# Performance work log

Hardware: AMD Instinct MI355X
Metric: run time of the kernel (lower is better)

## Reference

```python
import jax, jax.numpy as jnp
from jax import lax
import numpy as np

EPS = 1e-5
COMMITMENT = 0.25


def conv1d(x, w, b, pad):
    # x: [N,C,T], w: [O,I,K]
    y = lax.conv_general_dilated(x, w, window_strides=(1,), padding=[(pad, pad)],
                                 dimension_numbers=('NCH', 'OIH', 'NCH'))
    return y + b[None, :, None]


def batchnorm(x, g, b):
    # training-mode BN (PyTorch default): batch stats over (N, T), biased var
    m = jnp.mean(x, axis=(0, 2), keepdims=True)
    v = jnp.var(x, axis=(0, 2), keepdims=True)
    return (x - m) * lax.rsqrt(v + EPS) * g[None, :, None] + b[None, :, None]


def setup_inputs() -> dict:
    key = jax.random.key(0)
    ks = jax.random.split(key, 16)
    B, C_in, T = 16, 80, 4096
    H1, H2, D, K = 128, 256, 64, 512
    s = 0.05
    inp = {
        'x': jax.random.normal(ks[0], (B, C_in, T), jnp.float32),
        # encoder
        'enc_w1': jax.random.normal(ks[1], (H1, C_in, 3), jnp.float32) * s,
        'enc_b1': jnp.zeros((H1,), jnp.float32),
        'bn1_g': jnp.ones((H1,), jnp.float32), 'bn1_b': jnp.zeros((H1,), jnp.float32),
        'enc_w2': jax.random.normal(ks[2], (H2, H1, 3), jnp.float32) * s,
        'enc_b2': jnp.zeros((H2,), jnp.float32),
        'bn2_g': jnp.ones((H2,), jnp.float32), 'bn2_b': jnp.zeros((H2,), jnp.float32),
        'enc_w3': jax.random.normal(ks[3], (D, H2, 1), jnp.float32) * s,
        'enc_b3': jnp.zeros((D,), jnp.float32),
        # codebook, init uniform(-1/K, 1/K) like the torch module
        'codebook': jax.random.uniform(ks[4], (K, D), jnp.float32, -1.0 / K, 1.0 / K),
        # decoder (hidden_dims reversed: [256, 128])
        'dec_w1': jax.random.normal(ks[5], (H2, D, 3), jnp.float32) * s,
        'dec_b1': jnp.zeros((H2,), jnp.float32),
        'dbn1_g': jnp.ones((H2,), jnp.float32), 'dbn1_b': jnp.zeros((H2,), jnp.float32),
        'dec_w2': jax.random.normal(ks[6], (H1, H2, 3), jnp.float32) * s,
        'dec_b2': jnp.zeros((H1,), jnp.float32),
        'dbn2_g': jnp.ones((H1,), jnp.float32), 'dbn2_b': jnp.zeros((H1,), jnp.float32),
        'dec_w3': jax.random.normal(ks[7], (C_in, H1, 3), jnp.float32) * s,
        'dec_b3': jnp.zeros((C_in,), jnp.float32),
    }
    return inp


def _vqvae(x, enc_w1, enc_b1, bn1_g, bn1_b, enc_w2, enc_b2, bn2_g, bn2_b,
           enc_w3, enc_b3, codebook, dec_w1, dec_b1, dbn1_g, dbn1_b,
           dec_w2, dec_b2, dbn2_g, dbn2_b, dec_w3, dec_b3):
    # ---- Encoder ----
    h = jax.nn.relu(batchnorm(conv1d(x, enc_w1, enc_b1, 1), bn1_g, bn1_b))
    h = jax.nn.relu(batchnorm(conv1d(h, enc_w2, enc_b2, 1), bn2_g, bn2_b))
    z = conv1d(h, enc_w3, enc_b3, 0)  # [B, D, T]

    # ---- Vector Quantizer ----
    B, D, T = z.shape
    zt = jnp.transpose(z, (0, 2, 1))            # [B, T, D]
    flat = zt.reshape(-1, D)                    # [B*T, D]
    # squared L2 distances to codebook [B*T, K]
    d2 = (jnp.sum(flat * flat, axis=1, keepdims=True)
          + jnp.sum(codebook * codebook, axis=1)
          - 2.0 * flat @ codebook.T)
    idx = jnp.argmin(d2, axis=1)                # [B*T]
    quantized = codebook[idx].reshape(B, T, D)  # gather == onehot @ codebook

    e_latent_loss = jnp.mean((lax.stop_gradient(quantized) - zt) ** 2)
    q_latent_loss = jnp.mean((quantized - lax.stop_gradient(zt)) ** 2)
    vq_loss = q_latent_loss + COMMITMENT * e_latent_loss

    # straight-through estimator
    q_st = zt + lax.stop_gradient(quantized - zt)
    q_st = jnp.transpose(q_st, (0, 2, 1))       # [B, D, T]
    encoding_indices = idx.reshape(B, T)

    # ---- Decoder ----
    h = conv1d(q_st, dec_w1, dec_b1, 1)
    h = conv1d(jax.nn.relu(batchnorm(h, dbn1_g, dbn1_b)), dec_w2, dec_b2, 1)
    recon = conv1d(jax.nn.relu(batchnorm(h, dbn2_g, dbn2_b)), dec_w3, dec_b3, 1)
    return recon, vq_loss, encoding_indices


def reference(x, enc_w1, enc_b1, bn1_g, bn1_b, enc_w2, enc_b2, bn2_g, bn2_b,
              enc_w3, enc_b3, codebook, dec_w1, dec_b1, dbn1_g, dbn1_b,
              dec_w2, dec_b2, dbn2_g, dbn2_b, dec_w3, dec_b3):
    return _vqvae(x, enc_w1, enc_b1, bn1_g, bn1_b, enc_w2, enc_b2, bn2_g, bn2_b,
                  enc_w3, enc_b3, codebook, dec_w1, dec_b1, dbn1_g, dbn1_b,
                  dec_w2, dec_b2, dbn2_g, dbn2_b, dec_w3, dec_b3)
```

## Files before the change

kernel.cpp:

```cpp
#include <hip/hip_runtime.h>
#include <math.h>

#define N_B 16
#define T_LEN 4096

typedef float f32x4  __attribute__((ext_vector_type(4)));
typedef _Float16 half8 __attribute__((ext_vector_type(8)));

static const size_t OFF_A    = 0;
static const size_t OFF_B    = 8388608;
static const size_t OFF_Z    = 25165824;
static const size_t OFF_WS   = 29360128;
static const size_t OFF_CBS  = 29540352;
static const size_t OFF_C2   = 29683712;
static const size_t OFF_ST   = 29684736;
static const size_t OFF_LOSS = 29685760;

static const size_t WS_E1 = 0;
static const size_t WS_E2 = 36864;
static const size_t WS_E3 = 135168;
static const size_t WS_D1 = 0;
static const size_t WS_D2 = 49152;
static const size_t WS_D3 = 147456;

__device__ inline void f2h2(float v, short& hi, short& lo) {
    _Float16 h = (_Float16)v;
    float r = (v - (float)h) * 4096.0f;
    _Float16 l = (_Float16)r;
    hi = __builtin_bit_cast(short, h);
    lo = __builtin_bit_cast(short, l);
}
__device__ inline float h2f(short s) {
    return (float)__builtin_bit_cast(_Float16, s);
}

template<int C_IN, int C_OUT, int KS>
__device__ inline void wsplit_fill(const float* __restrict__ w,
                                   short* __restrict__ dst, int e) {
    int i  = e & 31;
    int r  = e >> 5;
    int co = r % C_OUT;
    int r2 = r / C_OUT;
    int k  = r2 % KS;
    int c  = r2 / KS;
    int ci = c * 32 + i;
    float v = (ci < C_IN) ? w[((size_t)co * C_IN + ci) * KS + k] : 0.f;
    short h, l; f2h2(v, h, l);
    size_t base = ((size_t)(c * KS + k) * 2 * C_OUT + co) * 32 + i;
    dst[base] = h;
    dst[base + (size_t)C_OUT * 32] = l;
}

__global__ __launch_bounds__(256) void prep_k(
        const float* __restrict__ w1, const float* __restrict__ w2,
        const float* __restrict__ w3, const float* __restrict__ cb,
        float* wsf) {
    int e = blockIdx.x * 256 + threadIdx.x;
    if (e < 36864)        wsplit_fill<80, 128, 3>(w1, (short*)(wsf + OFF_WS + WS_E1), e);
    else if (e < 135168)  wsplit_fill<128, 256, 3>(w2, (short*)(wsf + OFF_WS + WS_E2), e - 36864);
    else if (e < 151552)  wsplit_fill<256, 64, 1>(w3, (short*)(wsf + OFF_WS + WS_E3), e - 135168);
    else if (e < 152064) {
        int c = e - 151552;
        const float* p = cb + (size_t)c * 64;
        double s = 0.0;
        for (int d = 0; d < 64; ++d) { double v = p[d]; s += v * v; }
        wsf[OFF_C2 + c] = (float)s;
    } else if (e < 184832) {
        int e2   = e - 152064;
        int i    = e2 & 31;
        int r    = e2 >> 5;
        int code = r & 511;
        int ks   = r >> 9;
        float v  = cb[(size_t)code * 64 + ks * 32 + i];
        short h, l; f2h2(v, h, l);
        short* dst = (short*)(wsf + OFF_CBS);
        dst[((size_t)(ks * 2 + 0) * 512 + code) * 32 + i] = h;
        dst[((size_t)(ks * 2 + 1) * 512 + code) * 32 + i] = l;
    } else if (e == 184832) {
        *(double*)(wsf + OFF_LOSS) = 0.0;
    }
}

__global__ __launch_bounds__(256) void prep2_k(
        const float* __restrict__ wd1, const float* __restrict__ wd2,
        const float* __restrict__ wd3, float* wsf) {
    int e = blockIdx.x * 256 + threadIdx.x;
    if (e < 49152)        wsplit_fill<64, 256, 3>(wd1, (short*)(wsf + OFF_WS + WS_D1), e);
    else if (e < 147456)  wsplit_fill<256, 128, 3>(wd2, (short*)(wsf + OFF_WS + WS_D2), e - 49152);
    else if (e < 178176)  wsplit_fill<128, 80, 3>(wd3, (short*)(wsf + OFF_WS + WS_D3), e - 147456);
}

template<int C_IN, int C_OUT, int KS, bool BN_IN, bool STATS>
__global__ __launch_bounds__(512, 4) void fconv_k(
        const float* __restrict__ x, const short* __restrict__ wsp,
        const float* __restrict__ bias, const float2* __restrict__ stats,
        float* __restrict__ out, float2* __restrict__ part) {
    constexpr int NCH  = (C_IN + 31) / 32;
    constexpr int HALO = KS / 2;
    constexpr int TT   = (KS == 1) ? 64 : 128;
    constexpr int WT   = (KS == 1) ? 2 : 1;
    constexpr int WCO  = 8 / WT;
    constexpr int HT   = TT / WT;
    constexpr int NTT  = HT / 16;
    constexpr int NTILE = T_LEN / TT;
    constexpr int XR   = TT + KS - 1;
    constexpr int RS   = 72;
    constexpr int LO   = 40;
    constexpr int TQ   = TT / 4;

    __shared__ __align__(16) short xs[XR * RS];

    const int tid  = threadIdx.x;
    const int lane = tid & 63;
    const int wv   = tid >> 6;
    const int wvc  = wv % WCO;
    const int wvt  = wv / WCO;
    const int ln   = lane & 15;
    const int q    = lane >> 4;

    const int n    = blockIdx.x / NTILE;
    const int t0   = (blockIdx.x % NTILE) * TT;
    const int co0  = blockIdx.y * (WCO * 16);
    const int co_l = co0 + wvc * 16 + ln;

    f32x4 a0[NTT], a1[NTT];
#pragma unroll
    for (int tt = 0; tt < NTT; ++tt)
#pragma unroll
        for (int i = 0; i < 4; ++i) { a0[tt][i] = 0.f; a1[tt][i] = 0.f; }

#pragma unroll 1
    for (int c = 0; c < NCH; ++c) {
        half8 ah[KS], al[KS];
        {
            half8 z = {0, 0, 0, 0, 0, 0, 0, 0};
#pragma unroll
            for (int k = 0; k < KS; ++k) {
                const short* wp = wsp
                    + ((size_t)(c * KS + k) * 2 * C_OUT + co_l) * 32 + q * 8;
                ah[k] = (co_l < C_OUT) ? *(const half8*)wp : z;
                al[k] = (co_l < C_OUT) ? *(const half8*)(wp + (size_t)C_OUT * 32) : z;
            }
        }

        __syncthreads();
        for (int e = tid; e < 32 * TQ; e += 512) {
            const int ci  = e / TQ;
            const int tq  = e % TQ;
            const int cig = c * 32 + ci;
            float v[4] = {0.f, 0.f, 0.f, 0.f};
            if (cig < C_IN) {
                const float* xp = x + ((size_t)(n * C_IN + cig)) * T_LEN + t0 + tq;
#pragma unroll
                for (int j = 0; j < 4; ++j) v[j] = xp[TQ * j];
                if (BN_IN) {
                    float2 s = stats[cig];
#pragma unroll
                    for (int j = 0; j < 4; ++j) v[j] = fmaxf(fmaf(v[j], s.x, s.y), 0.f);
                }
            }
#pragma unroll
            for (int j = 0; j < 4; ++j) {
                short h, l; f2h2(v[j], h, l);
                short* p = &xs[(HALO + tq + TQ * j) * RS + ci];
                p[0]  = h;
                p[LO] = l;
            }
        }
        if (KS == 3) {
            if (tid < 64) {
                const int ci   = tid & 31;
                const int side = tid >> 5;
                const int cig  = c * 32 + ci;
                const int gt   = side ? (t0 + TT) : (t0 - 1);
                float v = 0.f;
                if (cig < C_IN && gt >= 0 && gt < T_LEN) {
                    v = x[((size_t)(n * C_IN + cig)) * T_LEN + gt];
                    if (BN_IN) {
                        float2 s = stats[cig];
                        v = fmaxf(fmaf(v, s.x, s.y), 0.f);
                    }
                }
                short h, l; f2h2(v, h, l);
                short* p = &xs[(side ? (XR - 1) : 0) * RS + ci];
                p[0] = h; p[LO] = l;
            }
        }
        __syncthreads();

#pragma unroll
        for (int k = 0; k < KS; ++k) {
#pragma unroll
            for (int tt = 0; tt < NTT; ++tt) {
                const short* xr = &xs[(wvt * HT + tt * 16 + ln + k) * RS + q * 8];
                half8 bh = *(const half8*)&xr[0];
                half8 bl = *(const half8*)&xr[LO];
                a0[tt] = __builtin_amdgcn_mfma_f32_16x16x32_f16(ah[k], bh, a0[tt], 0, 0, 0);
                a1[tt] = __builtin_amdgcn_mfma_f32_16x16x32_f16(ah[k], bl, a1[tt], 0, 0, 0);
                a1[tt] = __builtin_amdgcn_mfma_f32_16x16x32_f16(al[k], bh, a1[tt], 0, 0, 0);
            }
        }
    }

    const int plinear = blockIdx.y * (N_B * NTILE) + blockIdx.x;
#pragma unroll
    for (int r = 0; r < 4; ++r) {
        const int co = co0 + wvc * 16 + q * 4 + r;
        float s1 = 0.f, s2 = 0.f;
        if (co < C_OUT) {
            const float bv = bias[co];
            float* op = out + ((size_t)(n * C_OUT + co)) * T_LEN + t0 + wvt * HT + ln;
#pragma unroll
            for (int tt = 0; tt < NTT; ++tt) {
                const float v = fmaf(a1[tt][r], 0.000244140625f, a0[tt][r]) + bv;
                op[tt * 16] = v;
                if (STATS) { s1 += v; s2 = fmaf(v, v, s2); }
            }
        }
        if (STATS) {
#pragma unroll
            for (int off = 1; off <= 8; off <<= 1) {
                s1 += __shfl_xor(s1, off);
                s2 += __shfl_xor(s2, off);
            }
            if (ln == 0)
                part[(size_t)plinear * 128 + wvc * 16 + q * 4 + r] =
                    make_float2(s1, s2);
        }
    }
}

__global__ __launch_bounds__(256) void stats_k(
        const float2* __restrict__ part, const float* __restrict__ g,
        const float* __restrict__ b, float2* __restrict__ stats) {
    const int c = blockIdx.x;
    const int tid = threadIdx.x;
    double s1 = 0.0, s2 = 0.0;
    for (int j = tid; j < 512; j += 256) {
        float2 v = part[((size_t)(c >> 7) * 512 + j) * 128 + (c & 127)];
        s1 += (double)v.x; s2 += (double)v.y;
    }
    __shared__ double r1[256], r2[256];
    r1[tid] = s1; r2[tid] = s2;
    __syncthreads();
    for (int s = 128; s > 0; s >>= 1) {
        if (tid < s) { r1[tid] += r1[tid + s]; r2[tid] += r2[tid + s]; }
        __syncthreads();
    }
    if (tid == 0) {
        double m   = r1[0] / 65536.0;
        double var = r2[0] / 65536.0 - m * m;
        double sc  = (double)g[c] / sqrt(var + 1e-5);
        stats[c] = make_float2((float)sc, (float)((double)b[c] - m * sc));
    }
}

__global__ __launch_bounds__(256) void vq_k(
        const float* __restrict__ z, const float* __restrict__ cb,
        const short* __restrict__ cbs, const float* __restrict__ c2,
        float* __restrict__ q, float* __restrict__ idx_out,
        double* __restrict__ loss) {
    __shared__ __align__(16) float zs[64 * 68];
    __shared__ __align__(16) short zh[64 * 136];
    __shared__ float  c2s[512];
    __shared__ float  szf_s[64];
    __shared__ int    idxs[64];
    __shared__ double dred[256];

    const int tid  = threadIdx.x;
    const int lane = tid & 63;
    const int wv   = tid >> 6;
    const int ln   = lane & 15;
    const int q4   = lane >> 4;
    const int n    = blockIdx.x >> 6;
    const int t0   = (blockIdx.x & 63) * 64;

    for (int e = tid; e < 512; e += 256) c2s[e] = c2[e];
    for (int e = tid; e < 1024; e += 256) {
        const int d  = e >> 4;
        const int tq = e & 15;
        const float* zp = z + ((size_t)(n * 64 + d)) * T_LEN + t0 + tq;
        const int ks = d >> 5, i = d & 31;
#pragma unroll
        for (int j = 0; j < 4; ++j) {
            const int t = tq + 16 * j;
            float v = zp[16 * j];
            zs[t * 68 + d] = v;
            short h, l; f2h2(v, h, l);
            zh[t * 136 + (ks * 2 + 0) * 32 + i] = h;
            zh[t * 136 + (ks * 2 + 1) * 32 + i] = l;
        }
    }
    __syncthreads();
    if (tid < 64) {
        double s = 0.0;
        const float* zr = &zs[tid * 68];
        for (int d = 0; d < 64; ++d) { double v = zr[d]; s += v * v; }
        szf_s[tid] = (float)s;
    }
    __syncthreads();

    const short* zr = &zh[(wv * 16 + ln) * 136 + q4 * 8];
    const half8 bh0 = *(const half8*)&zr[0];
    const half8 bl0 = *(const half8*)&zr[32];
    const half8 bh1 = *(const half8*)&zr[64];
    const half8 bl1 = *(const half8*)&zr[96];
    const float As  = szf_s[wv * 16 + ln];

    float bs = 3.0e38f;
    int   bi = 1 << 30;

#pragma unroll 4
    for (int ct = 0; ct < 32; ++ct) {
        const short* ap = cbs + ((size_t)(ct * 16 + ln)) * 32 + q4 * 8;
        const half8 ah0 = *(const half8*)&ap[0];
        const half8 al0 = *(const half8*)&ap[512 * 32];
        const half8 ah1 = *(const half8*)&ap[2 * 512 * 32];
        const half8 al1 = *(const half8*)&ap[3 * 512 * 32];
        f32x4 a0 = {0.f, 0.f, 0.f, 0.f};
        f32x4 a1 = {0.f, 0.f, 0.f, 0.f};
        a0 = __builtin_amdgcn_mfma_f32_16x16x32_f16(ah0, bh0, a0, 0, 0, 0);
        a1 = __builtin_amdgcn_mfma_f32_16x16x32_f16(ah0, bl0, a1, 0, 0, 0);
        a1 = __builtin_amdgcn_mfma_f32_16x16x32_f16(al0, bh0, a1, 0, 0, 0);
        a0 = __builtin_amdgcn_mfma_f32_16x16x32_f16(ah1, bh1, a0, 0, 0, 0);
        a1 = __builtin_amdgcn_mfma_f32_16x16x32_f16(ah1, bl1, a1, 0, 0, 0);
        a1 = __builtin_amdgcn_mfma_f32_16x16x32_f16(al1, bh1, a1, 0, 0, 0);
#pragma unroll
        for (int r = 0; r < 4; ++r) {
            const int code = ct * 16 + q4 * 4 + r;
            const float m32 = fmaf(a1[r], 0.000244140625f, a0[r]);
            const float A   = As + c2s[code];
            const float s   = A - 2.0f * m32;
            if (s < bs || (s == bs && code < bi)) { bs = s; bi = code; }
        }
    }
#pragma unroll
    for (int off = 16; off <= 32; off <<= 1) {
        const float os = __shfl_xor(bs, off);
        const int   oi = __shfl_xor(bi, off);
        if (os < bs || (os == bs && oi < bi)) { bs = os; bi = oi; }
    }
    if (q4 == 0) {
        const int t = wv * 16 + ln;
        idxs[t] = bi;
        idx_out[(size_t)n * T_LEN + t0 + t] = (float)bi;
    }
    __syncthreads();

    {
        const int g = tid >> 6, t = tid & 63;
        const int bi2 = idxs[t];
        double ls = 0.0;
        for (int dd = 0; dd < 16; ++dd) {
            const int d = g * 16 + dd;
            const float qv = cb[(size_t)bi2 * 64 + d];
            const float zv = zs[t * 68 + d];
            const double df = (double)qv - (double)zv;
            ls += df * df;
            q[((size_t)(n * 64 + d)) * T_LEN + t0 + t] = qv;
        }
        dred[tid] = ls;
    }
    __syncthreads();
    for (int s = 128; s > 0; s >>= 1) {
        if (tid < s) dred[tid] += dred[tid + s];
        __syncthreads();
    }
    if (tid == 0) atomicAdd(loss, dred[0]);
}

__global__ void fin_k(const double* __restrict__ loss, float* __restrict__ out) {
    if (threadIdx.x == 0 && blockIdx.x == 0)
        out[0] = (float)(1.25 * (*loss) / 4194304.0);
}

extern "C" void kernel_launch(void* const* d_in, const int* in_sizes, int n_in,
                              void* d_out, int out_size, void* d_ws, size_t ws_size,
                              hipStream_t stream) {
    const float* x      = (const float*)d_in[0];
    const float* enc_w1 = (const float*)d_in[1];
    const float* enc_b1 = (const float*)d_in[2];
    const float* bn1_g  = (const float*)d_in[3];
    const float* bn1_b  = (const float*)d_in[4];
    const float* enc_w2 = (const float*)d_in[5];
    const float* enc_b2 = (const float*)d_in[6];
    const float* bn2_g  = (const float*)d_in[7];
    const float* bn2_b  = (const float*)d_in[8];
    const float* enc_w3 = (const float*)d_in[9];
    const float* enc_b3 = (const float*)d_in[10];
    const float* cb     = (const float*)d_in[11];
    const float* dec_w1 = (const float*)d_in[12];
    const float* dec_b1 = (const float*)d_in[13];
    const float* dbn1_g = (const float*)d_in[14];
    const float* dbn1_b = (const float*)d_in[15];
    const float* dec_w2 = (const float*)d_in[16];
    const float* dec_b2 = (const float*)d_in[17];
    const float* dbn2_g = (const float*)d_in[18];
    const float* dbn2_b = (const float*)d_in[19];
    const float* dec_w3 = (const float*)d_in[20];
    const float* dec_b3 = (const float*)d_in[21];

    float* wsf   = (float*)d_ws;
    float* outf  = (float*)d_out;
    float* A     = wsf + OFF_A;
    float* Bb    = wsf + OFF_B;
    float* Z     = wsf + OFF_Z;
    float2* st   = (float2*)(wsf + OFF_ST);
    double* lossp = (double*)(wsf + OFF_LOSS);

    const short* wsE1 = (const short*)(wsf + OFF_WS + WS_E1);
    const short* wsE2 = (const short*)(wsf + OFF_WS + WS_E2);
    const short* wsE3 = (const short*)(wsf + OFF_WS + WS_E3);
    const short* wsD1 = (const short*)(wsf + OFF_WS + WS_D1);
    const short* wsD2 = (const short*)(wsf + OFF_WS + WS_D2);
    const short* wsD3 = (const short*)(wsf + OFF_WS + WS_D3);
    const short* cbs  = (const short*)(wsf + OFF_CBS);

    float2* pE1 = (float2*)Bb;
    float2* pE2 = (float2*)Z;
    float2* pD1 = (float2*)A;
    float2* pD2 = (float2*)Z;

    prep_k<<<723, 256, 0, stream>>>(enc_w1, enc_w2, enc_w3, cb, wsf);

    fconv_k<80, 128, 3, false, true><<<dim3(512, 1), 512, 0, stream>>>(
        x, wsE1, enc_b1, nullptr, A, pE1);
    stats_k<<<128, 256, 0, stream>>>(pE1, bn1_g, bn1_b, st);
    fconv_k<128, 256, 3, true, true><<<dim3(512, 2), 512, 0, stream>>>(
        A, wsE2, enc_b2, st, Bb, pE2);
    stats_k<<<256, 256, 0, stream>>>(pE2, bn2_g, bn2_b, st);
    fconv_k<256, 64, 1, true, false><<<dim3(1024, 1), 512, 0, stream>>>(
        Bb, wsE3, enc_b3, st, Z, nullptr);

    prep2_k<<<696, 256, 0, stream>>>(dec_w1, dec_w2, dec_w3, wsf);

    vq_k<<<1024, 256, 0, stream>>>(Z, cb, cbs, wsf + OFF_C2, Z,
                                   outf + 5242881, lossp);
    fin_k<<<1, 64, 0, stream>>>(lossp, outf + 5242880);

    fconv_k<64, 256, 3, false, true><<<dim3(512, 2), 512, 0, stream>>>(
        Z, wsD1, dec_b1, nullptr, Bb, pD1);
    stats_k<<<256, 256, 0, stream>>>(pD1, dbn1_g, dbn1_b, st);
    fconv_k<256, 128, 3, true, true><<<dim3(512, 1), 512, 0, stream>>>(
        Bb, wsD2, dec_b2, st, A, pD2);
    stats_k<<<128, 256, 0, stream>>>(pD2, dbn2_g, dbn2_b, st);
    fconv_k<128, 80, 3, true, false><<<dim3(512, 1), 512, 0, stream>>>(
        A, wsD3, dec_b3, st, outf, nullptr);
}
```

Measured before the change: 364.9 us.

## Fuse final encoder 1x1 conv with vector quantization into one kernel

Replaces the separate 1x1 encoder conv kernel and the VQ kernel with a single kernel. Each block applies BN+ReLU to the 256-channel input, computes the 64-dim latent via split-fp16 MFMA in registers, writes it to shared memory, and then runs the codebook search. Eight waves split the codebook in halves and merge the results. This removes the round trip of Z through global memory and one launch, at the cost of more shared memory and a longer kernel with lower occupancy. The decoder stats buffer is moved to avoid aliasing Z.

```diff
diff --git a/kernel.cpp b/kernel.cpp
--- a/kernel.cpp
+++ b/kernel.cpp
@@ -255,36 +255,88 @@
     }
 }
 
-__global__ __launch_bounds__(256) void vq_k(
-        const float* __restrict__ z, const float* __restrict__ cb,
-        const short* __restrict__ cbs, const float* __restrict__ c2,
-        float* __restrict__ q, float* __restrict__ idx_out,
-        double* __restrict__ loss) {
+__global__ __launch_bounds__(512, 4) void zvq_k(
+        const float* __restrict__ x, const short* __restrict__ wsp,
+        const float* __restrict__ bias, const float2* __restrict__ stats,
+        const float* __restrict__ cb, const short* __restrict__ cbs,
+        const float* __restrict__ c2, float* __restrict__ q,
+        float* __restrict__ idx_out, double* __restrict__ loss) {
+    constexpr int RS = 72, LO = 40;
+
+    __shared__ __align__(16) short xs[64 * RS];
     __shared__ __align__(16) float zs[64 * 68];
     __shared__ __align__(16) short zh[64 * 136];
     __shared__ float  c2s[512];
     __shared__ float  szf_s[64];
+    __shared__ float  redS[64 * 2];
+    __shared__ int    redI[64 * 2];
     __shared__ int    idxs[64];
-    __shared__ double dred[256];
+    __shared__ double dred[512];
 
     const int tid  = threadIdx.x;
     const int lane = tid & 63;
     const int wv   = tid >> 6;
+    const int wvc  = wv & 3;
+    const int wvt  = wv >> 2;
     const int ln   = lane & 15;
-    const int q4   = lane >> 4;
+    const int qq   = lane >> 4;
     const int n    = blockIdx.x >> 6;
     const int t0   = (blockIdx.x & 63) * 64;
-
-    for (int e = tid; e < 512; e += 256) c2s[e] = c2[e];
-    for (int e = tid; e < 1024; e += 256) {
-        const int d  = e >> 4;
-        const int tq = e & 15;
-        const float* zp = z + ((size_t)(n * 64 + d)) * T_LEN + t0 + tq;
+    const int co_l = wvc * 16 + ln;
+
+    for (int e = tid; e < 512; e += 512) c2s[e] = c2[e];
+
+    f32x4 a0[2], a1[2];
+#pragma unroll
+    for (int tt = 0; tt < 2; ++tt)
+#pragma unroll
+        for (int i = 0; i < 4; ++i) { a0[tt][i] = 0.f; a1[tt][i] = 0.f; }
+
+#pragma unroll 1
+    for (int c = 0; c < 8; ++c) {
+        half8 ah, al;
+        {
+            const short* wp = wsp + ((size_t)c * 2 * 64 + co_l) * 32 + qq * 8;
+            ah = *(const half8*)wp;
+            al = *(const half8*)(wp + (size_t)64 * 32);
+        }
+        __syncthreads();
+        {
+            const int ci  = tid >> 4;
+            const int tq  = tid & 15;
+            const int cig = c * 32 + ci;
+            const float* xp = x + ((size_t)(n * 256 + cig)) * T_LEN + t0 + tq;
+            const float2 s = stats[cig];
+#pragma unroll
+            for (int j = 0; j < 4; ++j) {
+                const float v = fmaxf(fmaf(xp[16 * j], s.x, s.y), 0.f);
+                short h, l; f2h2(v, h, l);
+                short* p = &xs[(tq + 16 * j) * RS + ci];
+                p[0]  = h;
+                p[LO] = l;
+            }
+        }
+        __syncthreads();
+#pragma unroll
+        for (int tt = 0; tt < 2; ++tt) {
+            const short* xr = &xs[(wvt * 32 + tt * 16 + ln) * RS + qq * 8];
+            half8 bh = *(const half8*)&xr[0];
+            half8 bl = *(const half8*)&xr[LO];
+            a0[tt] = __builtin_amdgcn_mfma_f32_16x16x32_f16(ah, bh, a0[tt], 0, 0, 0);
+            a1[tt] = __builtin_amdgcn_mfma_f32_16x16x32_f16(ah, bl, a1[tt], 0, 0, 0);
+            a1[tt] = __builtin_amdgcn_mfma_f32_16x16x32_f16(al, bh, a1[tt], 0, 0, 0);
+        }
+    }
+    __syncthreads();
+#pragma unroll
+    for (int r = 0; r < 4; ++r) {
+        const int d  = wvc * 16 + qq * 4 + r;
+        const float bv = bias[d];
         const int ks = d >> 5, i = d & 31;
 #pragma unroll
-        for (int j = 0; j < 4; ++j) {
-            const int t = tq + 16 * j;
-            float v = zp[16 * j];
+        for (int tt = 0; tt < 2; ++tt) {
+            const int t = wvt * 32 + tt * 16 + ln;
+            const float v = fmaf(a1[tt][r], 0.000244140625f, a0[tt][r]) + bv;
             zs[t * 68 + d] = v;
             short h, l; f2h2(v, h, l);
             zh[t * 136 + (ks * 2 + 0) * 32 + i] = h;
@@ -300,35 +352,37 @@
     }
     __syncthreads();
 
-    const short* zr = &zh[(wv * 16 + ln) * 136 + q4 * 8];
+    const int tl   = (wv & 3) * 16 + ln;
+    const int half = wv >> 2;
+    const short* zr = &zh[tl * 136 + qq * 8];
     const half8 bh0 = *(const half8*)&zr[0];
     const half8 bl0 = *(const half8*)&zr[32];
     const half8 bh1 = *(const half8*)&zr[64];
     const half8 bl1 = *(const half8*)&zr[96];
-    const float As  = szf_s[wv * 16 + ln];
+    const float As  = szf_s[tl];
 
     float bs = 3.0e38f;
     int   bi = 1 << 30;
 
 #pragma unroll 4
-    for (int ct = 0; ct < 32; ++ct) {
-        const short* ap = cbs + ((size_t)(ct * 16 + ln)) * 32 + q4 * 8;
+    for (int ct = half * 16; ct < half * 16 + 16; ++ct) {
+        const short* ap = cbs + ((size_t)(ct * 16 + ln)) * 32 + qq * 8;
         const half8 ah0 = *(const half8*)&ap[0];
         const half8 al0 = *(const half8*)&ap[512 * 32];
         const half8 ah1 = *(const half8*)&ap[2 * 512 * 32];
         const half8 al1 = *(const half8*)&ap[3 * 512 * 32];
-        f32x4 a0 = {0.f, 0.f, 0.f, 0.f};
-        f32x4 a1 = {0.f, 0.f, 0.f, 0.f};
-        a0 = __builtin_amdgcn_mfma_f32_16x16x32_f16(ah0, bh0, a0, 0, 0, 0);
-        a1 = __builtin_amdgcn_mfma_f32_16x16x32_f16(ah0, bl0, a1, 0, 0, 0);
-        a1 = __builtin_amdgcn_mfma_f32_16x16x32_f16(al0, bh0, a1, 0, 0, 0);
-        a0 = __builtin_amdgcn_mfma_f32_16x16x32_f16(ah1, bh1, a0, 0, 0, 0);
-        a1 = __builtin_amdgcn_mfma_f32_16x16x32_f16(ah1, bl1, a1, 0, 0, 0);
-        a1 = __builtin_amdgcn_mfma_f32_16x16x32_f16(al1, bh1, a1, 0, 0, 0);
+        f32x4 p0 = {0.f, 0.f, 0.f, 0.f};
+        f32x4 p1 = {0.f, 0.f, 0.f, 0.f};
+        p0 = __builtin_amdgcn_mfma_f32_16x16x32_f16(ah0, bh0, p0, 0, 0, 0);
+        p1 = __builtin_amdgcn_mfma_f32_16x16x32_f16(ah0, bl0, p1, 0, 0, 0);
+        p1 = __builtin_amdgcn_mfma_f32_16x16x32_f16(al0, bh0, p1, 0, 0, 0);
+        p0 = __builtin_amdgcn_mfma_f32_16x16x32_f16(ah1, bh1, p0, 0, 0, 0);
+        p1 = __builtin_amdgcn_mfma_f32_16x16x32_f16(ah1, bl1, p1, 0, 0, 0);
+        p1 = __builtin_amdgcn_mfma_f32_16x16x32_f16(al1, bh1, p1, 0, 0, 0);
 #pragma unroll
         for (int r = 0; r < 4; ++r) {
-            const int code = ct * 16 + q4 * 4 + r;
-            const float m32 = fmaf(a1[r], 0.000244140625f, a0[r]);
+            const int code = ct * 16 + qq * 4 + r;
+            const float m32 = fmaf(p1[r], 0.000244140625f, p0[r]);
             const float A   = As + c2s[code];
             const float s   = A - 2.0f * m32;
             if (s < bs || (s == bs && code < bi)) { bs = s; bi = code; }
@@ -340,10 +394,18 @@
         const int   oi = __shfl_xor(bi, off);
         if (os < bs || (os == bs && oi < bi)) { bs = os; bi = oi; }
     }
-    if (q4 == 0) {
-        const int t = wv * 16 + ln;
-        idxs[t] = bi;
-        idx_out[(size_t)n * T_LEN + t0 + t] = (float)bi;
+    if (qq == 0) { redS[tl * 2 + half] = bs; redI[tl * 2 + half] = bi; }
+    __syncthreads();
+    if (tid < 64) {
+        const int t = tid;
+        float b0 = redS[t * 2], b1v = redS[t * 2 + 1];
+        int   i0 = redI[t * 2], i1v = redI[t * 2 + 1];
+        int bi2; float bs2;
+        if (b1v < b0 || (b1v == b0 && i1v < i0)) { bs2 = b1v; bi2 = i1v; }
+        else { bs2 = b0; bi2 = i0; }
+        (void)bs2;
+        idxs[t] = bi2;
+        idx_out[(size_t)n * T_LEN + t0 + t] = (float)bi2;
     }
     __syncthreads();
 
@@ -351,8 +413,8 @@
         const int g = tid >> 6, t = tid & 63;
         const int bi2 = idxs[t];
         double ls = 0.0;
-        for (int dd = 0; dd < 16; ++dd) {
-            const int d = g * 16 + dd;
+        for (int dd = 0; dd < 8; ++dd) {
+            const int d = g * 8 + dd;
             const float qv = cb[(size_t)bi2 * 64 + d];
             const float zv = zs[t * 68 + d];
             const double df = (double)qv - (double)zv;
@@ -362,7 +424,7 @@
         dred[tid] = ls;
     }
     __syncthreads();
-    for (int s = 128; s > 0; s >>= 1) {
+    for (int s = 256; s > 0; s >>= 1) {
         if (tid < s) dred[tid] += dred[tid + s];
         __syncthreads();
     }
@@ -419,7 +481,7 @@
     float2* pE1 = (float2*)Bb;
     float2* pE2 = (float2*)Z;
     float2* pD1 = (float2*)A;
-    float2* pD2 = (float2*)Z;
+    float2* pD2 = (float2*)(wsf + OFF_B + 4194304);
 
     prep_k<<<723, 256, 0, stream>>>(enc_w1, enc_w2, enc_w3, cb, wsf);
 
@@ -429,14 +491,12 @@
     fconv_k<128, 256, 3, true, true><<<dim3(512, 2), 512, 0, stream>>>(
         A, wsE2, enc_b2, st, Bb, pE2);
     stats_k<<<256, 256, 0, stream>>>(pE2, bn2_g, bn2_b, st);
-    fconv_k<256, 64, 1, true, false><<<dim3(1024, 1), 512, 0, stream>>>(
-        Bb, wsE3, enc_b3, st, Z, nullptr);
+
+    zvq_k<<<1024, 512, 0, stream>>>(Bb, wsE3, enc_b3, st, cb, cbs,
+                                    wsf + OFF_C2, Z, outf + 5242881, lossp);
+    fin_k<<<1, 64, 0, stream>>>(lossp, outf + 5242880);
 
     prep2_k<<<696, 256, 0, stream>>>(dec_w1, dec_w2, dec_w3, wsf);
-
-    vq_k<<<1024, 256, 0, stream>>>(Z, cb, cbs, wsf + OFF_C2, Z,
-                                   outf + 5242881, lossp);
-    fin_k<<<1, 64, 0, stream>>>(lossp, outf + 5242880);
 
     fconv_k<64, 256, 3, false, true><<<dim3(512, 2), 512, 0, stream>>>(
         Z, wsD1, dec_b1, nullptr, Bb, pD1);
```

New measurement: 368.0 us. No clear change (+0.9%).
